# Kernel optimization log

Measured on AMD Instinct MI355X. Metric: run time of the kernel, lower is better.

## Reference

```python
import jax, jax.numpy as jnp
import numpy as np

STRIDE = 1
PADDING = (1, 1, 1, 1)  # (left, right, top, bottom), as in torch F.pad for last two dims
NEG_INF = -jnp.inf


def maxplus_conv2d(x, kernel, stride=STRIDE):
    """Tropical (max-plus) conv2d, groups=1.
    x: [B, C, H, W] (already padded), kernel: [O, C, kh, kw].
    out[b,o,h,w] = max_{c,ki,kj} x[b,c,h*s+ki,w*s+kj] + kernel[o,c,ki,kj]
    """
    B, C, H, W = x.shape
    O, Cg, kh, kw = kernel.shape
    Ho = (H - kh) // stride + 1
    Wo = (W - kw) // stride + 1
    out = jnp.full((B, O, Ho, Wo), NEG_INF, dtype=x.dtype)
    # Loop over the small, fixed kernel taps (kh*kw = 9); reductions over the
    # channel axis stay fully vectorized and fuse into a single add+reduce-max.
    for ki in range(kh):
        for kj in range(kw):
            xs = x[:, :, ki:ki + Ho * stride:stride, kj:kj + Wo * stride:stride]  # [B,C,Ho,Wo]
            cand = jnp.max(xs[:, None, :, :, :] + kernel[None, :, :, ki, kj][:, :, :, None, None], axis=2)
            out = jnp.maximum(out, cand)
    return out


def setup_inputs() -> dict:
    key = jax.random.key(0)
    kx, kk = jax.random.split(key)
    x = jax.random.normal(kx, (8, 64, 64, 64), dtype=jnp.float32)
    kernel = jax.random.normal(kk, (64, 64, 3, 3), dtype=jnp.float32) * 0.1
    return {"x": x, "kernel": kernel}


def reference(x, kernel):
    left, right, top, bottom = PADDING
    # MaxPlus semifield: pad with the additive identity of max, i.e. -inf
    xp = jnp.pad(x, ((0, 0), (0, 0), (top, bottom), (left, right)), mode="constant", constant_values=NEG_INF)
    return maxplus_conv2d(xp, kernel, STRIDE)
```

## Files before the change

### kernel.cpp

```cpp
#include <hip/hip_runtime.h>

#define NEG_INF (-__builtin_huge_valf())

#define CCH   4
#define HB    4
#define ROWS  (HB + 2)
#define XSTR  64
#define ESTR  40
#define SLOTS 6

__global__ __launch_bounds__(64, 4)
void maxplus_conv2d_kernel(const float* __restrict__ x,
                           const float* __restrict__ kern,
                           float* __restrict__ out) {
    __shared__ float xs[CCH * ROWS * XSTR];
    __shared__ float es[CCH * ROWS * ESTR];

    const int tid = threadIdx.x;
    const int wg  = tid & 15;
    const int hr  = tid >> 4;
    const int w0  = wg << 2;

    const int h_base = blockIdx.x * HB;
    const int b      = blockIdx.y;
    const int o_base = blockIdx.z << 1;

    const float* xb = x + (size_t)b * 64 * 64 * 64;
    const float* gsrc[SLOTS];
    float*       xdst[SLOTS];
    float*       edst[SLOTS];
    bool         vmask[SLOTS];
#pragma unroll
    for (int k = 0; k < SLOTS; ++k) {
        int rowid = k * 4 + hr;
        int cl    = rowid / ROWS;
        int r     = rowid - cl * ROWS;
        int gh    = h_base + r - 1;
        bool valid = (unsigned)gh < 64u;
        int  ghc   = valid ? gh : 0;
        gsrc[k]  = xb + ((size_t)cl * 64 + ghc) * 64 + wg * 4;
        xdst[k]  = &xs[rowid * XSTR + wg * 4];
        edst[k]  = &es[rowid * ESTR + wg];
        vmask[k] = valid;
    }

    if (tid < CCH * ROWS) {
        es[tid * ESTR + 0]  = NEG_INF;
        es[tid * ESTR + 34] = NEG_INF;
    }

    float acc[2][4];
#pragma unroll
    for (int oo = 0; oo < 2; ++oo)
#pragma unroll
        for (int wi = 0; wi < 4; ++wi)
            acc[oo][wi] = NEG_INF;

    float4 R[SLOTS];
#pragma unroll
    for (int k = 0; k < SLOTS; ++k) R[k] = *(const float4*)gsrc[k];

#pragma unroll 1
    for (int cc = 0; cc < 64; cc += CCH) {
        __syncthreads();

#pragma unroll
        for (int k = 0; k < SLOTS; ++k) {
            float4 v = R[k];
            if (!vmask[k]) v = make_float4(NEG_INF, NEG_INF, NEG_INF, NEG_INF);
            *(float4*)xdst[k] = v;
            edst[k][1]  = v.w;
            edst[k][18] = v.x;
        }

        __syncthreads();

        if (cc + CCH < 64) {
#pragma unroll
            for (int k = 0; k < SLOTS; ++k) {
                gsrc[k] += CCH * 64 * 64;
                R[k] = *(const float4*)gsrc[k];
            }
        }

        float kv[CCH][2][9];
#pragma unroll
        for (int cl = 0; cl < CCH; ++cl)
#pragma unroll
            for (int oo = 0; oo < 2; ++oo) {
                const float* kp = kern + ((size_t)(o_base + oo) * 64 + (cc + cl)) * 9;
#pragma unroll
                for (int t = 0; t < 9; ++t) kv[cl][oo][t] = kp[t];
            }

#pragma unroll
        for (int cl = 0; cl < CCH; ++cl) {
            float xv[3][6];
#pragma unroll
            for (int r = 0; r < 3; ++r) {
                const int rowid = cl * ROWS + hr + r;
                float4 m = *(const float4*)(&xs[rowid * XSTR + w0]);
                const float* ep = &es[rowid * ESTR + wg];
                xv[r][0] = ep[0];
                xv[r][5] = ep[19];
                xv[r][1] = m.x; xv[r][2] = m.y; xv[r][3] = m.z; xv[r][4] = m.w;
            }

#pragma unroll
            for (int oo = 0; oo < 2; ++oo) {
                const float* k9 = kv[cl][oo];
#pragma unroll
                for (int wi = 0; wi < 4; ++wi) {
                    float m = acc[oo][wi];
                    float t0 = xv[0][wi + 0] + k9[0];
                    float t1 = xv[0][wi + 1] + k9[1];
                    m = fmaxf(m, fmaxf(t0, t1));
                    t0 = xv[0][wi + 2] + k9[2];
                    t1 = xv[1][wi + 0] + k9[3];
                    m = fmaxf(m, fmaxf(t0, t1));
                    t0 = xv[1][wi + 1] + k9[4];
                    t1 = xv[1][wi + 2] + k9[5];
                    m = fmaxf(m, fmaxf(t0, t1));
                    t0 = xv[2][wi + 0] + k9[6];
                    t1 = xv[2][wi + 1] + k9[7];
                    m = fmaxf(m, fmaxf(t0, t1));
                    m = fmaxf(m, xv[2][wi + 2] + k9[8]);
                    acc[oo][wi] = m;
                }
            }
        }
    }

    const int h = h_base + hr;
#pragma unroll
    for (int oo = 0; oo < 2; ++oo) {
        float4 v = make_float4(acc[oo][0], acc[oo][1], acc[oo][2], acc[oo][3]);
        *(float4*)(out + ((((size_t)b * 64 + (o_base + oo)) * 64 + h) * 64 + w0)) = v;
    }
}

extern "C" void kernel_launch(void* const* d_in, const int* in_sizes, int n_in,
                              void* d_out, int out_size, void* d_ws, size_t ws_size,
                              hipStream_t stream) {
    const float* x    = (const float*)d_in[0];
    const float* kern = (const float*)d_in[1];
    float* out = (float*)d_out;

    dim3 grid(16, 8, 32);
    dim3 block(64);
    maxplus_conv2d_kernel<<<grid, block, 0, stream>>>(x, kern, out);
}
```

Baseline: 109.8 us.

## Replace halo shared buffer with DPP lane shifts and packed fp32 adds

Drops the separate edge-halo shared array. The left and right neighbour columns now come from cross-lane DPP row shifts of the main row registers, with -inf filled at row edges. The add step is rewritten with 2-wide float vectors so the compiler can emit packed fp32 adds (v_pk_add_f32), halving the add instruction count. This removes the extra LDS stores and loads plus the halo init, at the cost of DPP dependencies and some register shuffling to form the vector pairs.

```diff
diff --git a/kernel.cpp b/kernel.cpp
--- a/kernel.cpp
+++ b/kernel.cpp
@@ -1,4 +1,6 @@
 #include <hip/hip_runtime.h>
+
+typedef float v2f __attribute__((ext_vector_type(2)));
 
 #define NEG_INF (-__builtin_huge_valf())
 
@@ -6,15 +8,22 @@
 #define HB    4
 #define ROWS  (HB + 2)
 #define XSTR  64
-#define ESTR  40
 #define SLOTS 6
+
+__device__ __forceinline__ float dpp_shr1(float v, float old) {
+    return __int_as_float(__builtin_amdgcn_update_dpp(
+        __float_as_int(old), __float_as_int(v), 0x111, 0xF, 0xF, false));
+}
+__device__ __forceinline__ float dpp_shl1(float v, float old) {
+    return __int_as_float(__builtin_amdgcn_update_dpp(
+        __float_as_int(old), __float_as_int(v), 0x101, 0xF, 0xF, false));
+}
 
 __global__ __launch_bounds__(64, 4)
 void maxplus_conv2d_kernel(const float* __restrict__ x,
                            const float* __restrict__ kern,
                            float* __restrict__ out) {
     __shared__ float xs[CCH * ROWS * XSTR];
-    __shared__ float es[CCH * ROWS * ESTR];
 
     const int tid = threadIdx.x;
     const int wg  = tid & 15;
@@ -28,7 +37,6 @@
     const float* xb = x + (size_t)b * 64 * 64 * 64;
     const float* gsrc[SLOTS];
     float*       xdst[SLOTS];
-    float*       edst[SLOTS];
     bool         vmask[SLOTS];
 #pragma unroll
     for (int k = 0; k < SLOTS; ++k) {
@@ -40,14 +48,10 @@
         int  ghc   = valid ? gh : 0;
         gsrc[k]  = xb + ((size_t)cl * 64 + ghc) * 64 + wg * 4;
         xdst[k]  = &xs[rowid * XSTR + wg * 4];
-        edst[k]  = &es[rowid * ESTR + wg];
         vmask[k] = valid;
     }
 
-    if (tid < CCH * ROWS) {
-        es[tid * ESTR + 0]  = NEG_INF;
-        es[tid * ESTR + 34] = NEG_INF;
-    }
+    const float ninf = NEG_INF;
 
     float acc[2][4];
 #pragma unroll
@@ -69,8 +73,6 @@
             float4 v = R[k];
             if (!vmask[k]) v = make_float4(NEG_INF, NEG_INF, NEG_INF, NEG_INF);
             *(float4*)xdst[k] = v;
-            edst[k][1]  = v.w;
-            edst[k][18] = v.x;
         }
 
         __syncthreads();
@@ -95,37 +97,33 @@
 
 #pragma unroll
         for (int cl = 0; cl < CCH; ++cl) {
-            float xv[3][6];
 #pragma unroll
             for (int r = 0; r < 3; ++r) {
                 const int rowid = cl * ROWS + hr + r;
                 float4 m = *(const float4*)(&xs[rowid * XSTR + w0]);
-                const float* ep = &es[rowid * ESTR + wg];
-                xv[r][0] = ep[0];
-                xv[r][5] = ep[19];
-                xv[r][1] = m.x; xv[r][2] = m.y; xv[r][3] = m.z; xv[r][4] = m.w;
-            }
+                float le = dpp_shr1(m.w, ninf);
+                float re = dpp_shl1(m.x, ninf);
+
+                v2f P0 = {le,  m.x};
+                v2f P1 = {m.y, m.z};
+                v2f P2 = {m.w, re };
+                v2f Q0 = {m.x, m.y};
+                v2f Q1 = {m.z, m.w};
 
 #pragma unroll
-            for (int oo = 0; oo < 2; ++oo) {
-                const float* k9 = kv[cl][oo];
-#pragma unroll
-                for (int wi = 0; wi < 4; ++wi) {
-                    float m = acc[oo][wi];
-                    float t0 = xv[0][wi + 0] + k9[0];
-                    float t1 = xv[0][wi + 1] + k9[1];
-                    m = fmaxf(m, fmaxf(t0, t1));
-                    t0 = xv[0][wi + 2] + k9[2];
-                    t1 = xv[1][wi + 0] + k9[3];
-                    m = fmaxf(m, fmaxf(t0, t1));
-                    t0 = xv[1][wi + 1] + k9[4];
-                    t1 = xv[1][wi + 2] + k9[5];
-                    m = fmaxf(m, fmaxf(t0, t1));
-                    t0 = xv[2][wi + 0] + k9[6];
-                    t1 = xv[2][wi + 1] + k9[7];
-                    m = fmaxf(m, fmaxf(t0, t1));
-                    m = fmaxf(m, xv[2][wi + 2] + k9[8]);
-                    acc[oo][wi] = m;
+                for (int oo = 0; oo < 2; ++oo) {
+                    const float* k9 = kv[cl][oo];
+                    v2f ka = {k9[3*r+0], k9[3*r+0]};
+                    v2f kb = {k9[3*r+1], k9[3*r+1]};
+                    v2f kc = {k9[3*r+2], k9[3*r+2]};
+                    v2f a0 = P0 + ka, b0 = P1 + ka;
+                    v2f a1 = Q0 + kb, b1 = Q1 + kb;
+                    v2f a2 = P1 + kc, b2 = P2 + kc;
+
+                    acc[oo][0] = fmaxf(acc[oo][0], fmaxf(fmaxf(a0.x, a1.x), a2.x));
+                    acc[oo][1] = fmaxf(acc[oo][1], fmaxf(fmaxf(a0.y, a1.y), a2.y));
+                    acc[oo][2] = fmaxf(acc[oo][2], fmaxf(fmaxf(b0.x, b1.x), b2.x));
+                    acc[oo][3] = fmaxf(acc[oo][3], fmaxf(fmaxf(b0.y, b1.y), b2.y));
                 }
             }
         }
```

Measured after the change: 110.6 us. No clear change (+0.7%).
